# Optimization experiments

Hardware: AMD Instinct MI355X
Metric: run time of the kernel (lower is better)

## Reference

```python
import jax, jax.numpy as jnp
import numpy as np

B, N, D = 4, 256, 256
H, DH = 4, 64
INNER = H * DH
L, MULT, EDGE, KNN = 2, 2, 11, 3
LN_EPS = 1e-5


def _layernorm(x, w, b):
    m = x.mean(-1, keepdims=True)
    v = ((x - m) ** 2).mean(-1, keepdims=True)
    return (x - m) * jax.lax.rsqrt(v + LN_EPS) * w + b


def _gelu(x):
    return jax.nn.gelu(x, approximate=False)  # torch nn.GELU default = exact erf


def _knn_pair_mask(coords, valid, k):
    # coords [B,M,2], valid [B,M] -> symmetric KNN adjacency among neighbors
    Bm, M = valid.shape
    d = jnp.sqrt(jnp.sum((coords[:, :, None, :] - coords[:, None, :, :]) ** 2, -1))
    eye = jnp.eye(M, dtype=bool)[None]
    inv = ~(valid[:, :, None] & valid[:, None, :])
    d = jnp.where(inv | eye, jnp.inf, d)
    neg, idx = jax.lax.top_k(-d, k)  # k smallest distances
    finite = jnp.isfinite(neg)
    bi = jnp.arange(Bm)[:, None, None]
    ri = jnp.arange(M)[None, :, None]
    mask = jnp.zeros((Bm, M, M), bool).at[bi, ri, idx].set(finite)
    mask = mask | jnp.swapaxes(mask, 1, 2)
    return mask & ~eye


def _build_graph(x, coords):
    # valid node mask (infer_valid_node_mask) and hop ids (infer_hop_ids)
    valid = (jnp.abs(x).sum(-1) > 0).at[:, 0].set(True)
    hop = jnp.ones((B, N), jnp.int32).at[:, 0].set(0)
    hop = hop.at[:, 1 + (N - 1) // 2:].set(2)
    eye = jnp.eye(N, dtype=bool)[None]
    adj = jnp.broadcast_to(eye, (B, N, N))
    nv = valid[:, 1:]
    adj = adj.at[:, 0, 1:].set(nv)
    adj = adj.at[:, 1:, 0].set(nv)
    npm = _knn_pair_mask(coords[:, 1:], nv, min(KNN, N - 2))
    adj = adj.at[:, 1:, 1:].set(adj[:, 1:, 1:] | npm)
    vp = valid[:, :, None] & valid[:, None, :]
    adj = adj & (vp | eye)
    # edge features [B,N,N,11]
    rel = coords[:, None, :, :] - coords[:, :, None, :]  # coords[j]-coords[i]
    dx, dy = rel[..., 0], rel[..., 1]
    dist = jnp.sqrt(dx ** 2 + dy ** 2 + 1e-8)
    cdist = jnp.sqrt(coords[..., 0] ** 2 + coords[..., 1] ** 2 + 1e-8)
    nvm = valid.at[:, 0].set(False)
    cd = jnp.where(nvm, cdist, 0.0)
    cnt = jnp.clip(nvm.sum(-1), 1).astype(x.dtype)
    ls = cd.sum(-1) / cnt
    ls = jnp.where(ls > 0, ls, 1.0)
    ndist = dist / jnp.clip(ls, 1e-6)[:, None, None]
    idx = jnp.arange(N)
    ones2 = jnp.ones((N, N), bool)
    qic = (idx[:, None] == 0) & ones2
    kic = (idx[None, :] == 0) & ones2
    eye2 = jnp.eye(N, dtype=bool)
    isnn = ~(qic | kic | eye2)
    same_hop = hop[:, :, None] == hop[:, None, :]
    hop_delta = jnp.abs(hop[:, None, :] - hop[:, :, None]).astype(x.dtype)
    same_ct = jnp.zeros((B, N, N), x.dtype)  # cell_inf is None
    f = lambda m: jnp.broadcast_to(m.astype(x.dtype), (B, N, N))
    edge_attr = jnp.stack(
        [dx, dy, dist, ndist, f(qic), f(kic), f(eye2), f(isnn),
         same_hop.astype(x.dtype), hop_delta, same_ct], -1)
    return adj, edge_attr


def _forward(x, coords, Wq, Wk, Wv, eb_w1, eb_b1, eb_w2, eb_b2,
             ev_w1, ev_b1, ev_w2, ev_b2, Wo, bo,
             ln1_w, ln1_b, ln2_w, ln2_b, ff_w1, ff_b1, ff_w2, ff_b2):
    adj, e = _build_graph(x, coords)
    scale = DH ** -0.5
    big = jnp.finfo(x.dtype).max
    for l in range(L):
        xn = _layernorm(x, ln1_w[l], ln1_b[l])
        q = (xn @ Wq[l]).reshape(B, N, H, DH).transpose(0, 2, 1, 3)  # b h n d
        k = (xn @ Wk[l]).reshape(B, N, H, DH).transpose(0, 2, 1, 3)
        v = (xn @ Wv[l]).reshape(B, N, H, DH).transpose(0, 2, 1, 3)
        eb = _gelu(e @ eb_w1[l] + eb_b1[l]) @ eb_w2[l] + eb_b2[l]  # [B,N,N,H]
        ev = _gelu(e @ ev_w1[l] + ev_b1[l]) @ ev_w2[l] + ev_b2[l]  # [B,N,N,INNER]
        ev = ev.reshape(B, N, N, H, DH).transpose(0, 3, 1, 2, 4)   # b h i j d
        sim = jnp.einsum('bhid,bhjd->bhij', q, k) * scale + eb.transpose(0, 3, 1, 2)
        sim = jnp.where(adj[:, None], sim, -big)
        attn = jax.nn.softmax(sim, -1)
        msgs = v[:, :, None, :, :] + ev                            # value injection
        out = jnp.einsum('bhij,bhijd->bhid', attn, msgs)
        out = out.transpose(0, 2, 1, 3).reshape(B, N, INNER) @ Wo[l] + bo[l]
        x = x + out
        xn2 = _layernorm(x, ln2_w[l], ln2_b[l])
        hg = xn2 @ ff_w1[l] + ff_b1[l]
        a, g = jnp.split(hg, 2, -1)  # GEGLU
        x = x + ((a * _gelu(g)) @ ff_w2[l] + ff_b2[l])
    return x


def setup_inputs() -> dict:
    key = jax.random.key(0)
    ks = iter(jax.random.split(key, 32))
    w = lambda shape, s=0.05: jax.random.normal(next(ks), shape, jnp.float32) * s
    return {
        'x': jax.random.normal(next(ks), (B, N, D), jnp.float32),
        'coords': jax.random.normal(next(ks), (B, N, 2), jnp.float32) * 3.0,
        'Wq': w((L, D, INNER)), 'Wk': w((L, D, INNER)), 'Wv': w((L, D, INNER)),
        'eb_w1': w((L, EDGE, INNER)), 'eb_b1': jnp.zeros((L, INNER)),
        'eb_w2': w((L, INNER, H)), 'eb_b2': jnp.zeros((L, H)),
        'ev_w1': w((L, EDGE, INNER)), 'ev_b1': jnp.zeros((L, INNER)),
        'ev_w2': w((L, INNER, INNER)), 'ev_b2': jnp.zeros((L, INNER)),
        'Wo': w((L, INNER, D)), 'bo': jnp.zeros((L, D)),
        'ln1_w': jnp.ones((L, D)), 'ln1_b': jnp.zeros((L, D)),
        'ln2_w': jnp.ones((L, D)), 'ln2_b': jnp.zeros((L, D)),
        'ff_w1': w((L, D, 2 * MULT * D)), 'ff_b1': jnp.zeros((L, 2 * MULT * D)),
        'ff_w2': w((L, MULT * D, D)), 'ff_b2': jnp.zeros((L, D)),
    }


def reference(x, coords, Wq, Wk, Wv, eb_w1, eb_b1, eb_w2, eb_b2,
              ev_w1, ev_b1, ev_w2, ev_b2, Wo, bo,
              ln1_w, ln1_b, ln2_w, ln2_b, ff_w1, ff_b1, ff_w2, ff_b2):
    return _forward(x, coords, Wq, Wk, Wv, eb_w1, eb_b1, eb_w2, eb_b2,
                    ev_w1, ev_b1, ev_w2, ev_b2, Wo, bo,
                    ln1_w, ln1_b, ln2_w, ln2_b, ff_w1, ff_b1, ff_w2, ff_b2)
```

## Files before the change

kernel.cpp:

```cpp
#include <hip/hip_runtime.h>


#define MAXE  16384
#define NONX  22080
#define BF16_TOTAL 1441792

typedef __attribute__((ext_vector_type(8))) short bf16x8;
typedef __attribute__((ext_vector_type(4))) float f32x4;

struct PtrPack { const void* p[23]; };

__device__ __forceinline__ float bf2f(unsigned short s) {
  return __uint_as_float(((unsigned)s) << 16);
}
__device__ __forceinline__ unsigned short f2bf(float f) {
  unsigned u = __float_as_uint(f);
  u += 0x7fffu + ((u >> 16) & 1u);
  return (unsigned short)(u >> 16);
}
__device__ __forceinline__ float gelu_f(float x) {
  return 0.5f * x * (1.0f + erff(x * 0.70710678118654752440f));
}
__device__ __forceinline__ float wave_red_sum(float v) {
#pragma unroll
  for (int o = 32; o > 0; o >>= 1) v += __shfl_xor(v, o);
  return v;
}

__device__ __forceinline__ void edge_feats(int i, int j, float cxi, float cyi,
                                           float cxj, float cyj, float lsd, float* e) {
  float dx = cxj - cxi, dy = cyj - cyi;
  float dist = sqrtf(dx * dx + dy * dy + 1e-8f);
  e[0] = dx; e[1] = dy; e[2] = dist; e[3] = dist / lsd;
  bool qic = (i == 0), kic = (j == 0), eye = (i == j);
  e[4] = qic ? 1.f : 0.f;
  e[5] = kic ? 1.f : 0.f;
  e[6] = eye ? 1.f : 0.f;
  e[7] = (!qic && !kic && !eye) ? 1.f : 0.f;
  int hi = (i == 0) ? 0 : ((i < 128) ? 1 : 2);
  int hj = (j == 0) ? 0 : ((j < 128) ? 1 : 2);
  e[8] = (hi == hj) ? 1.f : 0.f;
  int hd = hj - hi;
  e[9] = (float)(hd < 0 ? -hd : hd);
}

__global__ __launch_bounds__(256) void k_convert(PtrPack pp, float* __restrict__ blobF,
                                                 unsigned short* __restrict__ blobB,
                                                 int* __restrict__ valid,
                                                 float* __restrict__ rowsum,
                                                 int* __restrict__ gctr) {
  bool isf32 = (*(const unsigned*)pp.p[15] == 0x3F800000u);
  int t = threadIdx.x;
  if (blockIdx.x == 0 && t == 0) *gctr = 0;
  if (blockIdx.x < 1024) {
    if (blockIdx.x < 32) rowsum[blockIdx.x * 256 + t] = 0.f;
    int r = blockIdx.x;
    int idx = r * 256 + t;
    float v = isf32 ? ((const float*)pp.p[0])[idx]
                    : bf2f(((const unsigned short*)pp.p[0])[idx]);
    blobF[idx] = v;
    __shared__ float s[4];
    float a = wave_red_sum(fabsf(v));
    if ((t & 63) == 0) s[t >> 6] = a;
    __syncthreads();
    if (t == 0) valid[r] = ((s[0] + s[1] + s[2] + s[3]) > 0.0f) || ((r & 255) == 0);
  } else {
    const int fst[16] = {0,2048,7680,8192,10240,10304,15936,16448,16960,17472,17984,18496,19008,19520,21568,22080};
    const int fsz[15] = {2048,5632,512,2048,8,5632,512,512,512,512,512,512,512,2048,512};
    const int fin[15] = {1,5,6,7,8,9,10,12,14,15,16,17,18,20,22};
    const int bst[8]  = {0,131072,262144,393216,524288,655360,1179648,1441792};
    const int bin[7]  = {2,3,4,13,11,19,21};
    const int NUNITS = NONX + BF16_TOTAL / 4;
    for (int u = (blockIdx.x - 1024) * 256 + t; u < NUNITS; u += 1024 * 256) {
      if (u < NONX) {
        int s = 0;
        while (s < 14 && u >= fst[s + 1]) ++s;
        int e = u - fst[s];
        float v = 0.f;
        if (e < fsz[s]) v = isf32 ? ((const float*)pp.p[fin[s]])[e]
                                  : bf2f(((const unsigned short*)pp.p[fin[s]])[e]);
        blobF[262144 + u] = v;
      } else {
        int bi = (u - NONX) * 4;
        int s = 0;
        while (s < 6 && bi >= bst[s + 1]) ++s;
        int e = bi - bst[s];
        ushort4 o;
        if (isf32) {
          const float* sp = (const float*)pp.p[bin[s]] + e;
          o.x = f2bf(sp[0]); o.y = f2bf(sp[1]); o.z = f2bf(sp[2]); o.w = f2bf(sp[3]);
        } else {
          o = *(const ushort4*)((const unsigned short*)pp.p[bin[s]] + e);
        }
        *(ushort4*)&blobB[bi] = o;
      }
    }
  }
}

__global__ __launch_bounds__(256) void k_knn(const float* __restrict__ cf,
                                             const int* __restrict__ valid,
                                             int* __restrict__ knn) {
  int blk = blockIdx.x;
  int b = blk >> 6;
  int w = threadIdx.x >> 6, lane = threadIdx.x & 63;
  int i = (blk & 63) * 4 + w;
  const float2* cc = (const float2*)(cf + b * 512);
  float2 ci = cc[i];
  bool vi = (valid[b * 256 + i] != 0) && (i != 0);
  unsigned long long key[4];
#pragma unroll
  for (int k = 0; k < 4; ++k) {
    int j = lane + 64 * k;
    bool ok = vi && (j != 0) && (j != i) && (valid[b * 256 + j] != 0);
    unsigned long long kk = ~0ull;
    if (ok) {
      float2 cj = cc[j];
      float dx = ci.x - cj.x, dy = ci.y - cj.y;
      float dd = sqrtf(dx * dx + dy * dy);
      kk = (((unsigned long long)__float_as_uint(dd)) << 32) | (unsigned)j;
    }
    key[k] = kk;
  }
  int out[3];
#pragma unroll
  for (int rnd = 0; rnd < 3; ++rnd) {
    unsigned long long m = key[0];
    if (key[1] < m) m = key[1];
    if (key[2] < m) m = key[2];
    if (key[3] < m) m = key[3];
#pragma unroll
    for (int o = 32; o > 0; o >>= 1) {
      unsigned long long om = __shfl_xor(m, o);
      if (om < m) m = om;
    }
    out[rnd] = (m != ~0ull) ? (int)(m & 0xFFFFFFFFull) : -1;
#pragma unroll
    for (int k = 0; k < 4; ++k)
      if (key[k] == m) key[k] = ~0ull;
  }
  if (lane == 0) {
    knn[(b * 256 + i) * 3 + 0] = out[0];
    knn[(b * 256 + i) * 3 + 1] = out[1];
    knn[(b * 256 + i) * 3 + 2] = out[2];
  }
}

__global__ __launch_bounds__(256) void k_csr(const float* __restrict__ cf,
                                             const int* __restrict__ valid,
                                             const int* __restrict__ knn,
                                             float* __restrict__ lsbuf,
                                             int* __restrict__ deg, int* __restrict__ rowptr,
                                             int* __restrict__ rowof, int* __restrict__ colsb,
                                             int* __restrict__ gctr) {
  int b = blockIdx.x, t = threadIdx.x;
  __shared__ unsigned adjw[256][8];
  __shared__ float sred[8];
  __shared__ int wsum[4];
  __shared__ int sbase;

  int r = b * 256 + t;
  float cx = cf[r * 2 + 0], cy = cf[r * 2 + 1];
  int lv = valid[r];
#pragma unroll
  for (int w = 0; w < 8; ++w) adjw[t][w] = 0u;
  __syncthreads();

  atomicOr(&adjw[t][t >> 5], 1u << (t & 31));
  if (t >= 1 && lv) {
    atomicOr(&adjw[0][t >> 5], 1u << (t & 31));
    atomicOr(&adjw[t][0], 1u);
  }
#pragma unroll
  for (int s = 0; s < 3; ++s) {
    int j = knn[r * 3 + s];
    if (j >= 0) {
      atomicOr(&adjw[t][j >> 5], 1u << (j & 31));
      atomicOr(&adjw[j][t >> 5], 1u << (t & 31));
    }
  }
  float cdist = sqrtf(cx * cx + cy * cy + 1e-8f);
  int nvm = (t >= 1) && lv;
  float rs = wave_red_sum(nvm ? cdist : 0.0f);
  float rc = wave_red_sum(nvm ? 1.0f : 0.0f);
  if ((t & 63) == 0) { sred[t >> 6] = rs; sred[4 + (t >> 6)] = rc; }
  __syncthreads();

  if (t == 0) {
    float totd = sred[0] + sred[1] + sred[2] + sred[3];
    float totc = sred[4] + sred[5] + sred[6] + sred[7];
    float ls = totd / fmaxf(totc, 1.0f);
    ls = (ls > 0.0f) ? ls : 1.0f;
    lsbuf[b] = fmaxf(ls, 1e-6f);
  }

  int dg = 0;
#pragma unroll
  for (int w = 0; w < 8; ++w) dg += __popc(adjw[t][w]);

  int lane = t & 63, wv = t >> 6;
  int x = dg;
#pragma unroll
  for (int off = 1; off < 64; off <<= 1) {
    int y = __shfl_up(x, off);
    if (lane >= off) x += y;
  }
  if (lane == 63) wsum[wv] = x;
  __syncthreads();
  if (t == 0) sbase = atomicAdd(gctr, wsum[0] + wsum[1] + wsum[2] + wsum[3]);
  __syncthreads();
  int woff = 0;
#pragma unroll
  for (int k2 = 0; k2 < 4; ++k2) woff += (k2 < wv) ? wsum[k2] : 0;
  int off0 = sbase + woff + x - dg;

  rowptr[r] = off0;
  deg[r] = dg;
  int o = off0;
#pragma unroll
  for (int w = 0; w < 8; ++w) {
    unsigned bits = adjw[t][w];
    while (bits) {
      int bp = __ffs(bits) - 1;
      colsb[o] = w * 32 + bp;
      rowof[o] = r;
      ++o;
      bits &= bits - 1;
    }
  }
}

template <int AMODE, int OMODE>
__device__ __forceinline__ void mfma_body(const void* Aptr, int lda,
                                          const unsigned short* __restrict__ B, int ldb, int n0B,
                                          const float* __restrict__ bias,
                                          const float* resid,
                                          void* C, int ldc, int n0C,
                                          int m0, int K, bool obf,
                                          const float* __restrict__ lnG,
                                          const float* __restrict__ lnB) {
  __shared__ short As[16][72];
  __shared__ short Bs[64][72];
  __shared__ float sG[256], sB2[256];
  int t = threadIdx.x, lane = t & 63, w = t >> 6;

  int am = t >> 3, ak = (t & 7) * 8;
  int bk = t >> 2, bn = (t & 3) * 16;

  f32x4 acc;
  acc[0] = 0.f; acc[1] = 0.f; acc[2] = 0.f; acc[3] = 0.f;

  for (int kc = 0; kc < K; kc += 256) {
    bf16x8 aB[4];
    float4 aF[4][2];
    float4 gF[4][2];
    bf16x8 bR[4][2];
#pragma unroll
    for (int r = 0; r < 4; ++r) {
      int k0 = kc + r * 64;
      if (t < 128) {
        if (AMODE == 0) {
          aB[r] = *(const bf16x8*)((const unsigned short*)Aptr +
                                   (size_t)(m0 + am) * lda + k0 + ak);
        } else {
          const float* ap = (const float*)Aptr + (size_t)(m0 + am) * lda + k0 + ak;
          aF[r][0] = *(const float4*)ap;
          aF[r][1] = *(const float4*)(ap + 4);
          if (AMODE == 1) {
            gF[r][0] = *(const float4*)(ap + 512);
            gF[r][1] = *(const float4*)(ap + 516);
          }
        }
      }
      const unsigned short* bp = B + (size_t)(k0 + bk) * ldb + n0B + bn;
      bR[r][0] = *(const bf16x8*)bp;
      bR[r][1] = *(const bf16x8*)(bp + 8);
    }

    float mm = 0.f, rstd = 0.f;
    if (AMODE == 3) {
      sG[t] = lnG[t]; sB2[t] = lnB[t];
      if (t < 128) {
        float s = 0.f, ss = 0.f;
#pragma unroll
        for (int r = 0; r < 4; ++r)
#pragma unroll
          for (int h2 = 0; h2 < 2; ++h2) {
            float4 v4 = aF[r][h2];
            s += v4.x + v4.y + v4.z + v4.w;
            ss += v4.x * v4.x + v4.y * v4.y + v4.z * v4.z + v4.w * v4.w;
          }
        s += __shfl_xor(s, 1); s += __shfl_xor(s, 2); s += __shfl_xor(s, 4);
        ss += __shfl_xor(ss, 1); ss += __shfl_xor(ss, 2); ss += __shfl_xor(ss, 4);
        mm = s * (1.f / 256.f);
        float var = ss * (1.f / 256.f) - mm * mm;
        rstd = 1.f / sqrtf(var + 1e-5f);
      }
      __syncthreads();
    }

#pragma unroll
    for (int r = 0; r < 4; ++r) {
      if (t < 128) {
        if (AMODE == 0) {
          *(bf16x8*)&As[am][ak] = aB[r];
        } else if (AMODE == 1) {
          float4 a0 = aF[r][0], a1 = aF[r][1];
          float4 g0 = gF[r][0], g1 = gF[r][1];
          short tmp[8];
          tmp[0] = (short)f2bf(a0.x * gelu_f(g0.x));
          tmp[1] = (short)f2bf(a0.y * gelu_f(g0.y));
          tmp[2] = (short)f2bf(a0.z * gelu_f(g0.z));
          tmp[3] = (short)f2bf(a0.w * gelu_f(g0.w));
          tmp[4] = (short)f2bf(a1.x * gelu_f(g1.x));
          tmp[5] = (short)f2bf(a1.y * gelu_f(g1.y));
          tmp[6] = (short)f2bf(a1.z * gelu_f(g1.z));
          tmp[7] = (short)f2bf(a1.w * gelu_f(g1.w));
          *(bf16x8*)&As[am][ak] = *(bf16x8*)tmp;
        } else if (AMODE == 2) {
          float4 a0 = aF[r][0], a1 = aF[r][1];
          short tmp[8];
          tmp[0] = (short)f2bf(a0.x); tmp[1] = (short)f2bf(a0.y);
          tmp[2] = (short)f2bf(a0.z); tmp[3] = (short)f2bf(a0.w);
          tmp[4] = (short)f2bf(a1.x); tmp[5] = (short)f2bf(a1.y);
          tmp[6] = (short)f2bf(a1.z); tmp[7] = (short)f2bf(a1.w);
          *(bf16x8*)&As[am][ak] = *(bf16x8*)tmp;
        } else {
          float4 a0 = aF[r][0], a1 = aF[r][1];
          int kb = kc + r * 64 + ak;
          short tmp[8];
          tmp[0] = (short)f2bf((a0.x - mm) * rstd * sG[kb + 0] + sB2[kb + 0]);
          tmp[1] = (short)f2bf((a0.y - mm) * rstd * sG[kb + 1] + sB2[kb + 1]);
          tmp[2] = (short)f2bf((a0.z - mm) * rstd * sG[kb + 2] + sB2[kb + 2]);
          tmp[3] = (short)f2bf((a0.w - mm) * rstd * sG[kb + 3] + sB2[kb + 3]);
          tmp[4] = (short)f2bf((a1.x - mm) * rstd * sG[kb + 4] + sB2[kb + 4]);
          tmp[5] = (short)f2bf((a1.y - mm) * rstd * sG[kb + 5] + sB2[kb + 5]);
          tmp[6] = (short)f2bf((a1.z - mm) * rstd * sG[kb + 6] + sB2[kb + 6]);
          tmp[7] = (short)f2bf((a1.w - mm) * rstd * sG[kb + 7] + sB2[kb + 7]);
          *(bf16x8*)&As[am][ak] = *(bf16x8*)tmp;
        }
      }
      {
        bf16x8 bv0 = bR[r][0], bv1 = bR[r][1];
#pragma unroll
        for (int i2 = 0; i2 < 8; ++i2) Bs[bn + i2][bk] = bv0[i2];
#pragma unroll
        for (int i2 = 0; i2 < 8; ++i2) Bs[bn + 8 + i2][bk] = bv1[i2];
      }
      __syncthreads();
      int q = lane >> 4;
      bf16x8 af0 = *(const bf16x8*)&As[lane & 15][q * 8];
      bf16x8 af1 = *(const bf16x8*)&As[lane & 15][32 + q * 8];
      bf16x8 bf0 = *(const bf16x8*)&Bs[w * 16 + (lane & 15)][q * 8];
      bf16x8 bf1 = *(const bf16x8*)&Bs[w * 16 + (lane & 15)][32 + q * 8];
      acc = __builtin_amdgcn_mfma_f32_16x16x32_bf16(af0, bf0, acc, 0, 0, 0);
      acc = __builtin_amdgcn_mfma_f32_16x16x32_bf16(af1, bf1, acc, 0, 0, 0);
      __syncthreads();
    }
  }

  int q = lane >> 4;
  int cn = w * 16 + (lane & 15);
  int col = n0C + cn;
  float bv = bias ? bias[n0B + cn] : 0.0f;
#pragma unroll
  for (int rr = 0; rr < 4; ++rr) {
    int row = m0 + q * 4 + rr;
    float v = acc[rr] + bv;
    if (resid) v += resid[(size_t)row * ldc + col];
    if (OMODE == 2 || (OMODE == 1 && obf)) {
      ((unsigned short*)C)[(size_t)row * ldc + col] = f2bf(v);
    } else {
      ((float*)C)[(size_t)row * ldc + col] = v;
    }
  }
}

template <int AMODE, int OMODE>
__global__ __launch_bounds__(256) void k_mfma(const void* A, int lda, int aYoffBytes,
                                              const unsigned short* B, int ldb,
                                              const float* bias, const float* resid,
                                              void* C, int ldc, int K,
                                              const unsigned* probe,
                                              const float* lnG, const float* lnB) {
  bool obf = (OMODE == 1) && probe && (*probe != 0x3F800000u);
  int n0 = blockIdx.y * 64;
  const void* Ap = (const char*)A + (size_t)aYoffBytes * blockIdx.y;
  mfma_body<AMODE, OMODE>(Ap, lda, B, ldb, n0, bias, resid, C, ldc, n0,
                          blockIdx.x * 16, K, obf, lnG, lnB);
}

__global__ __launch_bounds__(256) void k_mfma_qkv(const float* X,
                                                  const float* lnG, const float* lnB,
                                                  const unsigned short* WqL, float* qkv) {
  int sel = blockIdx.y >> 2;
  const unsigned short* B = WqL + sel * 131072;
  int n0B = (blockIdx.y & 3) * 64;
  int n0C = blockIdx.y * 64;
  mfma_body<3, 0>(X, 256, B, 256, n0B, nullptr, nullptr, qkv, 768, n0C,
                  blockIdx.x * 16, 256, false, lnG, lnB);
}

__global__ __launch_bounds__(256) void k_simz(const float* __restrict__ cf,
                                              const float* __restrict__ qkv,
                                              const int* __restrict__ rowof,
                                              const int* __restrict__ colsb,
                                              const int* __restrict__ gctr,
                                              const float* __restrict__ lsbuf,
                                              const float* __restrict__ ebW1,
                                              const float* __restrict__ ebB1,
                                              const float* __restrict__ ebW2,
                                              const float* __restrict__ ebB2,
                                              float* __restrict__ esim,
                                              float* __restrict__ rowsum,
                                              float* __restrict__ tb,
                                              float* __restrict__ vs) {
  int t = threadIdx.x;
  {
    size_t tz = (size_t)blockIdx.x * 1024 + t;
    tb[tz] = 0.f; tb[tz + 256] = 0.f; tb[tz + 512] = 0.f; tb[tz + 768] = 0.f;
    vs[(size_t)blockIdx.x * 256 + t] = 0.f;
  }
  int E = *gctr;
  int lane = t & 63, w = t >> 6;
  float W1r[4][10], B1r[4], W2r[4][4];
#pragma unroll
  for (int kk = 0; kk < 4; ++kk) {
    int c = kk * 64 + lane;
    B1r[kk] = ebB1[c];
#pragma unroll
    for (int f = 0; f < 10; ++f) W1r[kk][f] = ebW1[f * 256 + c];
    float4 w2 = *(const float4*)(ebW2 + c * 4);
    W2r[kk][0] = w2.x; W2r[kk][1] = w2.y; W2r[kk][2] = w2.z; W2r[kk][3] = w2.w;
  }
  float b20 = ebB2[0], b21 = ebB2[1], b22 = ebB2[2], b23 = ebB2[3];
  for (int g = blockIdx.x * 4 + w; g < E; g += 4096) {
    int r = rowof[g], j = colsb[g];
    int b = r >> 8, i = r & 255;
    float ls = lsbuf[b];
    const float2* cc = (const float2*)cf;
    float2 ci = cc[b * 256 + i], cj = cc[b * 256 + j];
    float ef[10];
    edge_feats(i, j, ci.x, ci.y, cj.x, cj.y, ls, ef);
    float red[8];
#pragma unroll
    for (int z = 0; z < 8; ++z) red[z] = 0.0f;
#pragma unroll
    for (int kk = 0; kk < 4; ++kk) {
      int c = kk * 64 + lane;
      float h1 = B1r[kk];
#pragma unroll
      for (int f = 0; f < 10; ++f) h1 += ef[f] * W1r[kk][f];
      float g1 = gelu_f(h1);
      red[4] += g1 * W2r[kk][0];
      red[5] += g1 * W2r[kk][1];
      red[6] += g1 * W2r[kk][2];
      red[7] += g1 * W2r[kk][3];
      red[kk] = qkv[(size_t)r * 768 + c] * qkv[((size_t)(b * 256 + j)) * 768 + 256 + c];
    }
#pragma unroll
    for (int z = 0; z < 8; ++z) {
#pragma unroll
      for (int o = 32; o > 0; o >>= 1) red[z] += __shfl_xor(red[z], o);
    }
    if (lane == 0) {
      float e0 = expf(red[0] * 0.125f + red[4] + b20);
      float e1 = expf(red[1] * 0.125f + red[5] + b21);
      float e2 = expf(red[2] * 0.125f + red[6] + b22);
      float e3 = expf(red[3] * 0.125f + red[7] + b23);
      *(float4*)&esim[(size_t)g * 4] = make_float4(e0, e1, e2, e3);
      atomicAdd(&rowsum[r * 4 + 0], e0);
      atomicAdd(&rowsum[r * 4 + 1], e1);
      atomicAdd(&rowsum[r * 4 + 2], e2);
      atomicAdd(&rowsum[r * 4 + 3], e3);
    }
  }
}

__global__ __launch_bounds__(256, 4) void k_accum(const float* __restrict__ cf,
                                                  const float* __restrict__ qkv,
                                                  const int* __restrict__ rowptr,
                                                  const int* __restrict__ deg,
                                                  const int* __restrict__ colsb,
                                                  const float* __restrict__ esim,
                                                  const float* __restrict__ rowsum,
                                                  const float* __restrict__ lsbuf,
                                                  const float* __restrict__ evW1,
                                                  const float* __restrict__ evB1,
                                                  float* __restrict__ tb,
                                                  float* __restrict__ vs) {
  int x = blockIdx.x;
  int r, ch;
  if (x < 1024) { r = x; ch = 0; }
  else { int i5 = x - 1024; r = (i5 / 7) * 256; ch = 1 + i5 % 7; }
  int d = deg[r];
  int e0 = ch * 32;
  if (e0 >= d) return;
  int n = min(32, d - e0);
  int base = rowptr[r] + e0;
  int b = r >> 8, i = r & 255;
  int u = threadIdx.x, h = u >> 6;

  __shared__ int scols[32];
  __shared__ float4 sattn[32];
  __shared__ float sef[32][10];
  if (u < n) {
    float4 S4 = *(const float4*)&rowsum[r * 4];
    int j = colsb[base + u];
    scols[u] = j;
    float4 e = *(const float4*)&esim[(size_t)(base + u) * 4];
    sattn[u] = make_float4(e.x / S4.x, e.y / S4.y, e.z / S4.z, e.w / S4.w);
    float ls = lsbuf[b];
    const float2* cc = (const float2*)cf;
    float2 ci = cc[b * 256 + i], cj = cc[b * 256 + j];
    float ef[10];
    edge_feats(i, j, ci.x, ci.y, cj.x, cj.y, ls, ef);
#pragma unroll
    for (int f = 0; f < 10; ++f) sef[u][f] = ef[f];
  }
  __syncthreads();

  float evb = evB1[u];
  float w1r[10];
#pragma unroll
  for (int f = 0; f < 10; ++f) w1r[f] = evW1[f * 256 + u];
  float t0 = 0.f, t1 = 0.f, t2 = 0.f, t3 = 0.f, va = 0.f;
#pragma unroll 4
  for (int e = 0; e < n; ++e) {
    float4 a = sattn[e];
    int j = scols[e];
    float h1 = evb;
#pragma unroll
    for (int f = 0; f < 10; ++f) h1 += sef[e][f] * w1r[f];
    float g1 = gelu_f(h1);
    t0 += a.x * g1; t1 += a.y * g1; t2 += a.z * g1; t3 += a.w * g1;
    float ah = (h == 0) ? a.x : (h == 1) ? a.y : (h == 2) ? a.z : a.w;
    va += ah * qkv[((size_t)(b * 256 + j)) * 768 + 512 + u];
  }
  size_t tbase = (size_t)r * 1024 + u;
  atomicAdd(&tb[tbase], t0);
  atomicAdd(&tb[tbase + 256], t1);
  atomicAdd(&tb[tbase + 512], t2);
  atomicAdd(&tb[tbase + 768], t3);
  atomicAdd(&vs[(size_t)r * 256 + u], va);
}

extern "C" void kernel_launch(void* const* d_in, const int* in_sizes, int n_in,
                              void* d_out, int out_size, void* d_ws, size_t ws_size,
                              hipStream_t stream) {
  (void)in_sizes; (void)n_in; (void)out_size; (void)ws_size;

  char* wp = (char*)d_ws;
  auto carve = [&](size_t bytes) -> char* {
    char* p = wp;
    wp += ((bytes + 255) / 256) * 256;
    return p;
  };
  int*   gctr   = (int*)carve(4);
  float* lsb    = (float*)carve(16);
  int*   valid  = (int*)carve(1024 * 4);
  int*   deg    = (int*)carve(1024 * 4);
  int*   rowptr = (int*)carve(1024 * 4);
  int*   rowof  = (int*)carve(MAXE * 4);
  int*   colsb  = (int*)carve(MAXE * 4);
  int*   knn    = (int*)carve(1024 * 3 * 4);
  float* rowsum = (float*)carve(8192 * 4);
  float* sim    = (float*)carve((size_t)MAXE * 16);
  float* blobF  = (float*)carve((size_t)(262144 + NONX) * 4);
  unsigned short* blobB = (unsigned short*)carve((size_t)BF16_TOTAL * 2);
  float* qkv    = (float*)carve((size_t)1024 * 768 * 4);
  float* xcur   = (float*)carve((size_t)262144 * 4);
  float* tb     = (float*)carve((size_t)1048576 * 4);
  float* vs     = (float*)carve((size_t)262144 * 4);
  unsigned short* oi = (unsigned short*)carve((size_t)262144 * 2);

  const float* Xf    = blobF + 0;
  const float* Cf    = blobF + 262144;
  const float* ebW1  = blobF + 264192;
  const float* ebB1  = blobF + 269824;
  const float* ebW2  = blobF + 270336;
  const float* ebB2  = blobF + 272384;
  const float* evW1  = blobF + 272448;
  const float* evB1  = blobF + 278080;
  const float* evB2  = blobF + 278592;
  const float* boB   = blobF + 279104;
  const float* ln1w  = blobF + 279616;
  const float* ln1b  = blobF + 280128;
  const float* ln2w  = blobF + 280640;
  const float* ln2b  = blobF + 281152;
  const float* ffb1  = blobF + 281664;
  const float* ffb2  = blobF + 283712;
  const unsigned short* WqB   = blobB + 0;
  const unsigned short* WoB   = blobB + 393216;
  const unsigned short* evW2B = blobB + 524288;
  const unsigned short* ffw1B = blobB + 655360;
  const unsigned short* ffw2B = blobB + 1179648;

  PtrPack pp;
  for (int i = 0; i < 23; ++i) pp.p[i] = d_in[i];
  const unsigned* probe = (const unsigned*)d_in[15];

  k_convert<<<2048, 256, 0, stream>>>(pp, blobF, blobB, valid, rowsum, gctr);
  k_knn<<<256, 256, 0, stream>>>(Cf, valid, knn);
  k_csr<<<4, 256, 0, stream>>>(Cf, valid, knn, lsb, deg, rowptr, rowof, colsb, gctr);

  for (int l = 0; l < 2; ++l) {
    const float* xsrc = (l == 0) ? Xf : xcur;
    float* rsumL = rowsum + l * 4096;
    k_mfma_qkv<<<dim3(64, 12), 256, 0, stream>>>(xsrc, ln1w + l * 256, ln1b + l * 256,
                                                 WqB + l * 65536, qkv);
    k_simz<<<1024, 256, 0, stream>>>(Cf, qkv, rowof, colsb, gctr, lsb,
                                     ebW1 + l * 2816, ebB1 + l * 256,
                                     ebW2 + l * 1024, ebB2 + l * 4,
                                     sim, rsumL, tb, vs);
    k_accum<<<1052, 256, 0, stream>>>(Cf, qkv, rowptr, deg, colsb, sim, rsumL, lsb,
                                      evW1 + l * 2816, evB1 + l * 256, tb, vs);
    k_mfma<2, 2><<<dim3(64, 4), 256, 0, stream>>>(tb, 1024, 1024, evW2B + l * 65536, 256,
                                                  evB2 + l * 256, vs, oi, 256, 256,
                                                  nullptr, nullptr, nullptr);
    k_mfma<0, 0><<<dim3(64, 4), 256, 0, stream>>>(oi, 256, 0, WoB + l * 65536, 256,
                                                  boB + l * 256, xsrc, xcur, 256, 256,
                                                  nullptr, nullptr, nullptr);
    k_mfma<3, 0><<<dim3(64, 16), 256, 0, stream>>>(xcur, 256, 0, ffw1B + l * 262144, 1024,
                                                   ffb1 + l * 1024, nullptr, tb, 1024, 256,
                                                   nullptr, ln2w + l * 256, ln2b + l * 256);
    if (l == 0) {
      k_mfma<1, 0><<<dim3(64, 4), 256, 0, stream>>>(tb, 1024, 0, ffw2B + l * 131072, 256,
                                                    ffb2 + l * 256, xcur, xcur, 256, 512,
                                                    nullptr, nullptr, nullptr);
    } else {
      k_mfma<1, 1><<<dim3(64, 4), 256, 0, stream>>>(tb, 1024, 0, ffw2B + l * 131072, 256,
                                                    ffb2 + l * 256, xcur, d_out, 256, 512,
                                                    probe, nullptr, nullptr);
    }
  }
}
```

Measured before the change: 289.7 us.

## Fuse edge-score and accumulate kernels into one per-row attention kernel

Replaces the edge-parallel score kernel (global esim buffer plus rowsum atomics) and the chunked accumulate kernel with a single kernel that handles one query row per block. Scores are kept in shared memory and normalised with a block reduction, and outputs are written with plain stores, so the zero-fill, the atomics, the rowof/esim/rowsum buffers and one launch all go away. The cost is load imbalance: row 0 of each batch can have up to 256 neighbours and is now processed serially by a single block instead of being split into chunks.

```diff
diff --git a/kernel.cpp b/kernel.cpp
--- a/kernel.cpp
+++ b/kernel.cpp
@@ -47,13 +47,11 @@
 __global__ __launch_bounds__(256) void k_convert(PtrPack pp, float* __restrict__ blobF,
                                                  unsigned short* __restrict__ blobB,
                                                  int* __restrict__ valid,
-                                                 float* __restrict__ rowsum,
                                                  int* __restrict__ gctr) {
   bool isf32 = (*(const unsigned*)pp.p[15] == 0x3F800000u);
   int t = threadIdx.x;
   if (blockIdx.x == 0 && t == 0) *gctr = 0;
   if (blockIdx.x < 1024) {
-    if (blockIdx.x < 32) rowsum[blockIdx.x * 256 + t] = 0.f;
     int r = blockIdx.x;
     int idx = r * 256 + t;
     float v = isf32 ? ((const float*)pp.p[0])[idx]
@@ -151,7 +149,7 @@
                                              const int* __restrict__ knn,
                                              float* __restrict__ lsbuf,
                                              int* __restrict__ deg, int* __restrict__ rowptr,
-                                             int* __restrict__ rowof, int* __restrict__ colsb,
+                                             int* __restrict__ colsb,
                                              int* __restrict__ gctr) {
   int b = blockIdx.x, t = threadIdx.x;
   __shared__ unsigned adjw[256][8];
@@ -223,7 +221,6 @@
     while (bits) {
       int bp = __ffs(bits) - 1;
       colsb[o] = w * 32 + bp;
-      rowof[o] = r;
       ++o;
       bits &= bits - 1;
     }
@@ -401,28 +398,51 @@
                   blockIdx.x * 16, 256, false, lnG, lnB);
 }
 
-__global__ __launch_bounds__(256) void k_simz(const float* __restrict__ cf,
-                                              const float* __restrict__ qkv,
-                                              const int* __restrict__ rowof,
-                                              const int* __restrict__ colsb,
-                                              const int* __restrict__ gctr,
-                                              const float* __restrict__ lsbuf,
-                                              const float* __restrict__ ebW1,
-                                              const float* __restrict__ ebB1,
-                                              const float* __restrict__ ebW2,
-                                              const float* __restrict__ ebB2,
-                                              float* __restrict__ esim,
-                                              float* __restrict__ rowsum,
-                                              float* __restrict__ tb,
-                                              float* __restrict__ vs) {
-  int t = threadIdx.x;
-  {
-    size_t tz = (size_t)blockIdx.x * 1024 + t;
-    tb[tz] = 0.f; tb[tz + 256] = 0.f; tb[tz + 512] = 0.f; tb[tz + 768] = 0.f;
-    vs[(size_t)blockIdx.x * 256 + t] = 0.f;
-  }
-  int E = *gctr;
-  int lane = t & 63, w = t >> 6;
+__global__ __launch_bounds__(256, 2) void k_attn(const float* __restrict__ cf,
+                                                 const float* __restrict__ qkv,
+                                                 const int* __restrict__ rowptr,
+                                                 const int* __restrict__ deg,
+                                                 const int* __restrict__ colsb,
+                                                 const float* __restrict__ lsbuf,
+                                                 const float* __restrict__ ebW1,
+                                                 const float* __restrict__ ebB1,
+                                                 const float* __restrict__ ebW2,
+                                                 const float* __restrict__ ebB2,
+                                                 const float* __restrict__ evW1,
+                                                 const float* __restrict__ evB1,
+                                                 float* __restrict__ tb,
+                                                 float* __restrict__ vs) {
+  int r = blockIdx.x;
+  int b = r >> 8, i = r & 255;
+  int d = deg[r];
+  int base = rowptr[r];
+  int u = threadIdx.x, lane = u & 63, w = u >> 6;
+
+  __shared__ int scols[256];
+  __shared__ float4 sattn[256];
+  __shared__ float sef[256][10];
+  __shared__ float ssum[4][4];
+  __shared__ float sinv[4];
+
+  float ls = lsbuf[b];
+  const float2* cc = (const float2*)cf;
+  float2 ci = cc[b * 256 + i];
+
+  if (u < d) {
+    int j = colsb[base + u];
+    scols[u] = j;
+    float2 cj = cc[b * 256 + j];
+    float ef[10];
+    edge_feats(i, j, ci.x, ci.y, cj.x, cj.y, ls, ef);
+#pragma unroll
+    for (int f = 0; f < 10; ++f) sef[u][f] = ef[f];
+  }
+  __syncthreads();
+
+  float Qreg[4];
+#pragma unroll
+  for (int kk = 0; kk < 4; ++kk)
+    Qreg[kk] = qkv[(size_t)r * 768 + kk * 64 + lane];
   float W1r[4][10], B1r[4], W2r[4][4];
 #pragma unroll
   for (int kk = 0; kk < 4; ++kk) {
@@ -434,14 +454,11 @@
     W2r[kk][0] = w2.x; W2r[kk][1] = w2.y; W2r[kk][2] = w2.z; W2r[kk][3] = w2.w;
   }
   float b20 = ebB2[0], b21 = ebB2[1], b22 = ebB2[2], b23 = ebB2[3];
-  for (int g = blockIdx.x * 4 + w; g < E; g += 4096) {
-    int r = rowof[g], j = colsb[g];
-    int b = r >> 8, i = r & 255;
-    float ls = lsbuf[b];
-    const float2* cc = (const float2*)cf;
-    float2 ci = cc[b * 256 + i], cj = cc[b * 256 + j];
-    float ef[10];
-    edge_feats(i, j, ci.x, ci.y, cj.x, cj.y, ls, ef);
+
+  float s0 = 0.f, s1 = 0.f, s2 = 0.f, s3 = 0.f;
+  for (int e = w; e < d; e += 4) {
+    int j = scols[e];
+    const float* Kj = qkv + (size_t)(b * 256 + j) * 768 + 256;
     float red[8];
 #pragma unroll
     for (int z = 0; z < 8; ++z) red[z] = 0.0f;
@@ -450,84 +467,44 @@
       int c = kk * 64 + lane;
       float h1 = B1r[kk];
 #pragma unroll
-      for (int f = 0; f < 10; ++f) h1 += ef[f] * W1r[kk][f];
+      for (int f = 0; f < 10; ++f) h1 += sef[e][f] * W1r[kk][f];
       float g1 = gelu_f(h1);
       red[4] += g1 * W2r[kk][0];
       red[5] += g1 * W2r[kk][1];
       red[6] += g1 * W2r[kk][2];
       red[7] += g1 * W2r[kk][3];
-      red[kk] = qkv[(size_t)r * 768 + c] * qkv[((size_t)(b * 256 + j)) * 768 + 256 + c];
+      red[kk] = Qreg[kk] * Kj[c];
     }
 #pragma unroll
     for (int z = 0; z < 8; ++z) {
 #pragma unroll
       for (int o = 32; o > 0; o >>= 1) red[z] += __shfl_xor(red[z], o);
     }
-    if (lane == 0) {
-      float e0 = expf(red[0] * 0.125f + red[4] + b20);
-      float e1 = expf(red[1] * 0.125f + red[5] + b21);
-      float e2 = expf(red[2] * 0.125f + red[6] + b22);
-      float e3 = expf(red[3] * 0.125f + red[7] + b23);
-      *(float4*)&esim[(size_t)g * 4] = make_float4(e0, e1, e2, e3);
-      atomicAdd(&rowsum[r * 4 + 0], e0);
-      atomicAdd(&rowsum[r * 4 + 1], e1);
-      atomicAdd(&rowsum[r * 4 + 2], e2);
-      atomicAdd(&rowsum[r * 4 + 3], e3);
-    }
-  }
-}
-
-__global__ __launch_bounds__(256, 4) void k_accum(const float* __restrict__ cf,
-                                                  const float* __restrict__ qkv,
-                                                  const int* __restrict__ rowptr,
-                                                  const int* __restrict__ deg,
-                                                  const int* __restrict__ colsb,
-                                                  const float* __restrict__ esim,
-                                                  const float* __restrict__ rowsum,
-                                                  const float* __restrict__ lsbuf,
-                                                  const float* __restrict__ evW1,
-                                                  const float* __restrict__ evB1,
-                                                  float* __restrict__ tb,
-                                                  float* __restrict__ vs) {
-  int x = blockIdx.x;
-  int r, ch;
-  if (x < 1024) { r = x; ch = 0; }
-  else { int i5 = x - 1024; r = (i5 / 7) * 256; ch = 1 + i5 % 7; }
-  int d = deg[r];
-  int e0 = ch * 32;
-  if (e0 >= d) return;
-  int n = min(32, d - e0);
-  int base = rowptr[r] + e0;
-  int b = r >> 8, i = r & 255;
-  int u = threadIdx.x, h = u >> 6;
-
-  __shared__ int scols[32];
-  __shared__ float4 sattn[32];
-  __shared__ float sef[32][10];
-  if (u < n) {
-    float4 S4 = *(const float4*)&rowsum[r * 4];
-    int j = colsb[base + u];
-    scols[u] = j;
-    float4 e = *(const float4*)&esim[(size_t)(base + u) * 4];
-    sattn[u] = make_float4(e.x / S4.x, e.y / S4.y, e.z / S4.z, e.w / S4.w);
-    float ls = lsbuf[b];
-    const float2* cc = (const float2*)cf;
-    float2 ci = cc[b * 256 + i], cj = cc[b * 256 + j];
-    float ef[10];
-    edge_feats(i, j, ci.x, ci.y, cj.x, cj.y, ls, ef);
-#pragma unroll
-    for (int f = 0; f < 10; ++f) sef[u][f] = ef[f];
+    float e0 = expf(red[0] * 0.125f + red[4] + b20);
+    float e1 = expf(red[1] * 0.125f + red[5] + b21);
+    float e2 = expf(red[2] * 0.125f + red[6] + b22);
+    float e3 = expf(red[3] * 0.125f + red[7] + b23);
+    if (lane == 0) sattn[e] = make_float4(e0, e1, e2, e3);
+    s0 += e0; s1 += e1; s2 += e2; s3 += e3;
+  }
+  if (lane == 0) {
+    ssum[w][0] = s0; ssum[w][1] = s1; ssum[w][2] = s2; ssum[w][3] = s3;
   }
   __syncthreads();
-
+  if (u < 4) sinv[u] = 1.0f / (ssum[0][u] + ssum[1][u] + ssum[2][u] + ssum[3][u]);
+  __syncthreads();
+
+  float4 si = make_float4(sinv[0], sinv[1], sinv[2], sinv[3]);
   float evb = evB1[u];
   float w1r[10];
 #pragma unroll
   for (int f = 0; f < 10; ++f) w1r[f] = evW1[f * 256 + u];
+  int h = u >> 6;
   float t0 = 0.f, t1 = 0.f, t2 = 0.f, t3 = 0.f, va = 0.f;
 #pragma unroll 4
-  for (int e = 0; e < n; ++e) {
+  for (int e = 0; e < d; ++e) {
     float4 a = sattn[e];
+    a.x *= si.x; a.y *= si.y; a.z *= si.z; a.w *= si.w;
     int j = scols[e];
     float h1 = evb;
 #pragma unroll
@@ -538,11 +515,11 @@
     va += ah * qkv[((size_t)(b * 256 + j)) * 768 + 512 + u];
   }
   size_t tbase = (size_t)r * 1024 + u;
-  atomicAdd(&tb[tbase], t0);
-  atomicAdd(&tb[tbase + 256], t1);
-  atomicAdd(&tb[tbase + 512], t2);
-  atomicAdd(&tb[tbase + 768], t3);
-  atomicAdd(&vs[(size_t)r * 256 + u], va);
+  tb[tbase]       = t0;
+  tb[tbase + 256] = t1;
+  tb[tbase + 512] = t2;
+  tb[tbase + 768] = t3;
+  vs[(size_t)r * 256 + u] = va;
 }
 
 extern "C" void kernel_launch(void* const* d_in, const int* in_sizes, int n_in,
@@ -561,11 +538,8 @@
   int*   valid  = (int*)carve(1024 * 4);
   int*   deg    = (int*)carve(1024 * 4);
   int*   rowptr = (int*)carve(1024 * 4);
-  int*   rowof  = (int*)carve(MAXE * 4);
   int*   colsb  = (int*)carve(MAXE * 4);
   int*   knn    = (int*)carve(1024 * 3 * 4);
-  float* rowsum = (float*)carve(8192 * 4);
-  float* sim    = (float*)carve((size_t)MAXE * 16);
   float* blobF  = (float*)carve((size_t)(262144 + NONX) * 4);
   unsigned short* blobB = (unsigned short*)carve((size_t)BF16_TOTAL * 2);
   float* qkv    = (float*)carve((size_t)1024 * 768 * 4);
@@ -600,21 +574,18 @@
   for (int i = 0; i < 23; ++i) pp.p[i] = d_in[i];
   const unsigned* probe = (const unsigned*)d_in[15];
 
-  k_convert<<<2048, 256, 0, stream>>>(pp, blobF, blobB, valid, rowsum, gctr);
+  k_convert<<<2048, 256, 0, stream>>>(pp, blobF, blobB, valid, gctr);
   k_knn<<<256, 256, 0, stream>>>(Cf, valid, knn);
-  k_csr<<<4, 256, 0, stream>>>(Cf, valid, knn, lsb, deg, rowptr, rowof, colsb, gctr);
+  k_csr<<<4, 256, 0, stream>>>(Cf, valid, knn, lsb, deg, rowptr, colsb, gctr);
 
   for (int l = 0; l < 2; ++l) {
     const float* xsrc = (l == 0) ? Xf : xcur;
-    float* rsumL = rowsum + l * 4096;
     k_mfma_qkv<<<dim3(64, 12), 256, 0, stream>>>(xsrc, ln1w + l * 256, ln1b + l * 256,
                                                  WqB + l * 65536, qkv);
-    k_simz<<<1024, 256, 0, stream>>>(Cf, qkv, rowof, colsb, gctr, lsb,
+    k_attn<<<1024, 256, 0, stream>>>(Cf, qkv, rowptr, deg, colsb, lsb,
                                      ebW1 + l * 2816, ebB1 + l * 256,
                                      ebW2 + l * 1024, ebB2 + l * 4,
-                                     sim, rsumL, tb, vs);
-    k_accum<<<1052, 256, 0, stream>>>(Cf, qkv, rowptr, deg, colsb, sim, rsumL, lsb,
-                                      evW1 + l * 2816, evB1 + l * 256, tb, vs);
+                                     evW1 + l * 2816, evB1 + l * 256, tb, vs);
     k_mfma<2, 2><<<dim3(64, 4), 256, 0, stream>>>(tb, 1024, 1024, evW2B + l * 65536, 256,
                                                   evB2 + l * 256, vs, oi, 256, 256,
                                                   nullptr, nullptr, nullptr);
```

Measured after the change: 678.9 us. 2.34x slower.
